# Kernel optimization log

Measured on AMD Instinct MI355X. Metric: run time of the kernel, lower is better.

Reference implementation:

```python
import jax, jax.numpy as jnp
import numpy as np

B, S, D = 128, 144, 1024  # batch, grid tokens (12x12), d_model
GRID = 12


def _relative_position(grid_size):
    # Reconstructs get_grids_pos for a grid_size x grid_size grid of unit cells
    # (x_min = cell col/row index, x_max = x_min + 1), standard grid-feature layout.
    x = jnp.arange(grid_size, dtype=jnp.float32)
    px_min = jnp.repeat(x, grid_size)          # (S,) varies slowly (rows)
    py_min = jnp.tile(x, grid_size)            # (S,) varies fast (cols)
    px_max = px_min + 1.0
    py_max = py_min + 1.0
    cx = (px_min + px_max) * 0.5
    cy = (py_min + py_max) * 0.5
    w = px_max - px_min + 1.0                  # == 2 everywhere
    h = py_max - py_min + 1.0
    eps = 1e-10
    dx = jnp.log(jnp.maximum(jnp.abs((cx[:, None] - cx[None, :]) / w[:, None]), eps))
    dy = jnp.log(jnp.maximum(jnp.abs((cy[:, None] - cy[None, :]) / h[:, None]), eps))
    dw = jnp.log(w[:, None] / w[None, :])
    dh = jnp.log(h[:, None] / h[None, :])
    return jnp.stack([dx, dy, dw, dh], axis=-1)  # (S, S, 4)


def setup_inputs() -> dict:
    key = jax.random.key(0)
    ks = jax.random.split(key, 12)
    std = 0.02
    return {
        "query": jax.random.normal(ks[0], (B, S, D), jnp.float32),
        "key":   jax.random.normal(ks[1], (B, S, D), jnp.float32),
        "value": jax.random.normal(ks[2], (B, S, D), jnp.float32),
        # Linear weights stored as (in, out): y = x @ W + b
        "Wq": jax.random.normal(ks[3], (D, D), jnp.float32) * std,
        "bq": jnp.zeros((D,), jnp.float32),
        "Wk": jax.random.normal(ks[4], (D, D), jnp.float32) * std,
        "bk": jnp.zeros((D,), jnp.float32),
        "Wv": jax.random.normal(ks[5], (D, D), jnp.float32) * std,
        "bv": jnp.zeros((D,), jnp.float32),
        "Wl": jax.random.normal(ks[6], (4, D), jnp.float32) * std,
        "bl": jnp.zeros((D,), jnp.float32),
        "w_g": jax.random.normal(ks[7], (S, D, 1), jnp.float32) * std,
    }


def reference(query, key, value, Wq, bq, Wk, bk, Wv, bv, Wl, bl, w_g):
    d_model = query.shape[-1]
    scale = d_model ** (-0.5)
    act = jax.nn.relu  # get_activation_function() assumed relu; dropout=0 (eval)

    q = act(query @ Wq + bq)   # (B,S,D)
    k = act(key @ Wk + bk)
    v = act(value @ Wv + bv)

    attn = jnp.einsum('bid,bjd->bij', q, k) * scale  # (B,S,S)

    seq = value.shape[1]
    pos = _relative_position(int(round(seq ** 0.5)))  # (S,S,4)
    rel = act(pos @ Wl + bl)                          # (S,S,D)
    # torch.matmul(rela_pos, w_g): row i of the grid uses w_g[i]
    bias = act(jnp.einsum('ijd,id->ij', rel, w_g[..., 0]))  # (S,S)

    attn = jax.nn.softmax(attn + bias[None, :, :], axis=-1)
    return jnp.einsum('bij,bjd->bid', attn, v)
```

## Files before the change

### kernel.cpp

```cpp
#include <hip/hip_runtime.h>
#include <hip/hip_bf16.h>
#include <stdint.h>

#define SS 144
#define DD 1024
#define NB 128
#define SP 160
#define SCALE 0.03125f

typedef __attribute__((ext_vector_type(8))) short short8;
typedef __attribute__((ext_vector_type(4))) float floatx4;
typedef unsigned short u16;

#define MFMA(a, b, c) __builtin_amdgcn_mfma_f32_16x16x32_bf16((a), (b), (c), 0, 0, 0)

__device__ __forceinline__ u16 f2bf(float f) {
    union { float f; unsigned int i; } v; v.f = f;
    unsigned int r = v.i + 0x7fff + ((v.i >> 16) & 1);
    return (u16)(r >> 16);
}
__device__ __forceinline__ short8 pack8(float4 a, float4 b) {
    short8 r;
    r[0] = (short)f2bf(a.x); r[1] = (short)f2bf(a.y);
    r[2] = (short)f2bf(a.z); r[3] = (short)f2bf(a.w);
    r[4] = (short)f2bf(b.x); r[5] = (short)f2bf(b.y);
    r[6] = (short)f2bf(b.z); r[7] = (short)f2bf(b.w);
    return r;
}

__device__ __forceinline__ void gload16(u16* lds, const u16* g) {
    __builtin_amdgcn_global_load_lds(
        (__attribute__((address_space(1))) void*)g,
        (__attribute__((address_space(3))) void*)lds, 16, 0, 0);
}

__global__ __launch_bounds__(256) void convert_k(const float* __restrict__ X,
                                                 u16* __restrict__ O, int nchunk) {
    for (int c = blockIdx.x * 256 + threadIdx.x; c < nchunk; c += gridDim.x * 256) {
        size_t i = (size_t)c * 8;
        float4 a = *(const float4*)(X + i);
        float4 b = *(const float4*)(X + i + 4);
        *(short8*)(O + i) = pack8(a, b);
    }
}

__global__ void transpose_w_k(const float* __restrict__ Wq, const float* __restrict__ Wk,
                              const float* __restrict__ Wv, u16* __restrict__ WT) {
    __shared__ u16 t[32][33];
    int z = blockIdx.z;
    const float* W = z == 0 ? Wq : (z == 1 ? Wk : Wv);
    u16* O = WT + (size_t)z * DD * DD;
    int bn = blockIdx.x * 32, bk = blockIdx.y * 32;
    int tx = threadIdx.x & 31, ty = threadIdx.x >> 5;
    for (int r = ty; r < 32; r += 8) t[r][tx] = f2bf(W[(size_t)(bk + r) * DD + bn + tx]);
    __syncthreads();
    for (int r = ty; r < 32; r += 8) O[(size_t)(bn + r) * DD + bk + tx] = t[tx][r];
}

__global__ void bias_k(const float* __restrict__ Wl, const float* __restrict__ bl,
                       const float* __restrict__ wg, float* __restrict__ biasb) {
    int ij = blockIdx.x;
    int i = ij / SS, j = ij - i * SS;
    int lane = threadIdx.x;
    int ri = i / 12, ci = i - ri * 12, rj = j / 12, cj = j - rj * 12;
    float dx = logf(fmaxf(fabsf((float)(ri - rj)) * 0.5f, 1e-10f));
    float dy = logf(fmaxf(fabsf((float)(ci - cj)) * 0.5f, 1e-10f));
    float s = 0.f;
    for (int d = lane; d < DD; d += 64) {
        float r = dx * Wl[d] + dy * Wl[DD + d] + bl[d];
        r = fmaxf(r, 0.f);
        s += r * wg[(size_t)i * DD + d];
    }
    #pragma unroll
    for (int m = 32; m > 0; m >>= 1) s += __shfl_xor(s, m);
    if (lane == 0) biasb[ij] = fmaxf(s, 0.f);
}

__global__ __launch_bounds__(256) void proj_k(
    const u16* __restrict__ Xb, const u16* __restrict__ Wt,
    const float* __restrict__ bias,
    u16* __restrict__ O, u16* __restrict__ OvT, int z) {
    __shared__ __align__(16) u16 As[128 * 32];
    __shared__ __align__(16) u16 Bs[128 * 32];
    int bm = blockIdx.x, bn = blockIdx.y;
    int tid = threadIdx.x, lane = tid & 63, wv = tid >> 6;
    int wm = wv >> 1, wn = wv & 1;
    int lr = lane & 15, lq = lane >> 4;

    floatx4 zero4 = {0.f, 0.f, 0.f, 0.f};
    floatx4 acc[4][4];
    #pragma unroll
    for (int r = 0; r < 4; r++)
        #pragma unroll
        for (int c = 0; c < 4; c++) acc[r][c] = zero4;

    const u16* Abase = Xb + (size_t)bm * 128 * DD;
    const u16* Bbase = Wt + (size_t)bn * 128 * DD;

    int c0 = tid, c1 = tid + 256;
    const u16* ga0 = Abase + (size_t)(c0 >> 2) * DD + ((c0 & 3) << 3);
    const u16* ga1 = Abase + (size_t)(c1 >> 2) * DD + ((c1 & 3) << 3);
    const u16* gb0 = Bbase + (size_t)(c0 >> 2) * DD + ((c0 & 3) << 3);
    const u16* gb1 = Bbase + (size_t)(c1 >> 2) * DD + ((c1 & 3) << 3);
    u16* la0 = &As[c0 * 8];
    u16* la1 = &As[c1 * 8];
    u16* lb0 = &Bs[c0 * 8];
    u16* lb1 = &Bs[c1 * 8];

    for (int k0 = 0; k0 < DD; k0 += 32) {
        __syncthreads();
        gload16(la0, ga0 + k0);
        gload16(la1, ga1 + k0);
        gload16(lb0, gb0 + k0);
        gload16(lb1, gb1 + k0);
        __syncthreads();
        short8 a[4], b[4];
        #pragma unroll
        for (int r = 0; r < 4; r++)
            a[r] = *(const short8*)&As[(wm * 64 + r * 16 + lr) * 32 + lq * 8];
        #pragma unroll
        for (int c = 0; c < 4; c++)
            b[c] = *(const short8*)&Bs[(wn * 64 + c * 16 + lr) * 32 + lq * 8];
        #pragma unroll
        for (int r = 0; r < 4; r++)
            #pragma unroll
            for (int c = 0; c < 4; c++)
                acc[r][c] = MFMA(a[r], b[c], acc[r][c]);
    }

    int mrow0 = bm * 128 + wm * 64;
    int ncol0 = bn * 128 + wn * 64;
    if (z < 2) {
        #pragma unroll
        for (int r = 0; r < 4; r++)
            #pragma unroll
            for (int c = 0; c < 4; c++) {
                int col = ncol0 + c * 16 + lr;
                float bb = bias[col];
                #pragma unroll
                for (int i = 0; i < 4; i++) {
                    int row = mrow0 + r * 16 + lq * 4 + i;
                    O[(size_t)row * DD + col] = f2bf(fmaxf(acc[r][c][i] + bb, 0.f));
                }
            }
    } else {
        #pragma unroll
        for (int r = 0; r < 4; r++)
            #pragma unroll
            for (int c = 0; c < 4; c++) {
                int col = ncol0 + c * 16 + lr;
                float bb = bias[col];
                #pragma unroll
                for (int i = 0; i < 4; i++) {
                    int row = mrow0 + r * 16 + lq * 4 + i;
                    int bidx = row / SS;
                    int srow = row - bidx * SS;
                    OvT[((size_t)bidx * DD + col) * SP + srow] =
                        f2bf(fmaxf(acc[r][c][i] + bb, 0.f));
                }
            }
    }
}

__global__ __launch_bounds__(256) void attn_k(
    const u16* __restrict__ q, const u16* __restrict__ k,
    const float* __restrict__ biasb, u16* __restrict__ probs) {
    __shared__ float Sst[16][148];
    int it = blockIdx.x, b = blockIdx.y;
    int i0 = it * 16;
    int tid = threadIdx.x, lane = tid & 63, wv = tid >> 6;
    int lr = lane & 15, lq = lane >> 4;
    const u16* qs = q + ((size_t)b * SS + i0) * DD;
    const u16* ks = k + (size_t)b * SS * DD;

    floatx4 zero4 = {0.f, 0.f, 0.f, 0.f};
    floatx4 acc[3] = {zero4, zero4, zero4};
    int nt = (wv == 0) ? 3 : 2;

    for (int d0 = 0; d0 < DD; d0 += 32) {
        short8 a = *(const short8*)&qs[(size_t)lr * DD + d0 + lq * 8];
        #pragma unroll
        for (int m = 0; m < 3; m++) {
            if (m < nt) {
                int t = wv + m * 4;
                short8 bb = *(const short8*)&ks[(size_t)(t * 16 + lr) * DD + d0 + lq * 8];
                acc[m] = MFMA(a, bb, acc[m]);
            }
        }
    }
    for (int m = 0; m < nt; m++) {
        int t = wv + m * 4;
        #pragma unroll
        for (int i = 0; i < 4; i++) {
            int row = lq * 4 + i, col = t * 16 + lr;
            Sst[row][col] = acc[m][i] * SCALE + biasb[(i0 + row) * SS + col];
        }
    }
    __syncthreads();

    int g = tid >> 4, j = tid & 15;
    float mx = -1e30f;
    for (int c = j; c < SS; c += 16) mx = fmaxf(mx, Sst[g][c]);
    #pragma unroll
    for (int m = 1; m < 16; m <<= 1) mx = fmaxf(mx, __shfl_xor(mx, m));
    float sm = 0.f;
    float ev[9];
    int t = 0;
    for (int c = j; c < SS; c += 16, t++) { float e = expf(Sst[g][c] - mx); ev[t] = e; sm += e; }
    #pragma unroll
    for (int m = 1; m < 16; m <<= 1) sm += __shfl_xor(sm, m);
    float inv = 1.f / sm;
    u16* pr = probs + ((size_t)b * SS + i0 + g) * SP;
    t = 0;
    for (int c = j; c < SP; c += 16, t++) {
        float val = (c < SS) ? ev[t < 9 ? t : 8] * inv : 0.f;
        pr[c] = f2bf(val);
    }
}

__global__ __launch_bounds__(256) void pv_k(
    const u16* __restrict__ probs, const u16* __restrict__ vT, float* __restrict__ out) {
    int cb = blockIdx.x, it = blockIdx.y, b = blockIdx.z;
    int tid = threadIdx.x, lane = tid & 63, wv = tid >> 6;
    int lr = lane & 15, lq = lane >> 4;
    const u16* pr = probs + ((size_t)b * SS + it * 16) * SP;
    const u16* vt = vT + (size_t)b * DD * SP;
    int col0 = cb * 256 + wv * 64;

    floatx4 zero4 = {0.f, 0.f, 0.f, 0.f};
    floatx4 acc[4] = {zero4, zero4, zero4, zero4};
    for (int k0 = 0; k0 < SP; k0 += 32) {
        short8 a = *(const short8*)&pr[(size_t)lr * SP + k0 + lq * 8];
        #pragma unroll
        for (int c = 0; c < 4; c++) {
            short8 bb = *(const short8*)&vt[(size_t)(col0 + c * 16 + lr) * SP + k0 + lq * 8];
            acc[c] = MFMA(a, bb, acc[c]);
        }
    }
    #pragma unroll
    for (int c = 0; c < 4; c++)
        #pragma unroll
        for (int i = 0; i < 4; i++) {
            int row = it * 16 + lq * 4 + i, col = col0 + c * 16 + lr;
            out[((size_t)b * SS + row) * DD + col] = acc[c][i];
        }
}

extern "C" void kernel_launch(void* const* d_in, const int* in_sizes, int n_in,
                              void* d_out, int out_size, void* d_ws, size_t ws_size,
                              hipStream_t stream) {
    const float* query = (const float*)d_in[0];
    const float* key_  = (const float*)d_in[1];
    const float* value = (const float*)d_in[2];
    const float* Wq = (const float*)d_in[3];
    const float* bq = (const float*)d_in[4];
    const float* Wk = (const float*)d_in[5];
    const float* bk = (const float*)d_in[6];
    const float* Wv = (const float*)d_in[7];
    const float* bv = (const float*)d_in[8];
    const float* Wl = (const float*)d_in[9];
    const float* bl = (const float*)d_in[10];
    const float* wg = (const float*)d_in[11];

    u16* WT    = (u16*)d_ws;
    u16* Xbf   = WT + (size_t)3 * DD * DD;
    u16* q     = Xbf + (size_t)NB * SS * DD;
    u16* k     = q  + (size_t)NB * SS * DD;
    u16* vT    = k  + (size_t)NB * SS * DD;
    u16* probs = vT + (size_t)NB * DD * SP;
    float* biasb = (float*)(probs + (size_t)NB * SS * SP);

    transpose_w_k<<<dim3(32, 32, 3), 256, 0, stream>>>(Wq, Wk, Wv, WT);
    bias_k<<<dim3(SS * SS), 64, 0, stream>>>(Wl, bl, wg, biasb);

    const float* Xs[3] = {query, key_, value};
    const float* bs[3] = {bq, bk, bv};
    int nchunk = NB * SS * DD / 8;
    for (int z = 0; z < 3; z++) {
        convert_k<<<dim3(2048), 256, 0, stream>>>(Xs[z], Xbf, nchunk);
        proj_k<<<dim3(144, 8), 256, 0, stream>>>(Xbf, WT + (size_t)z * DD * DD, bs[z],
                                                 z == 0 ? q : k, vT, z);
    }
    attn_k<<<dim3(9, NB), 256, 0, stream>>>(q, k, biasb, probs);
    pv_k<<<dim3(4, 9, NB), 256, 0, stream>>>(probs, vT, (float*)d_out);
}
```

Before: 646.6 us.

## Double-buffer LDS tiles in projection GEMM and transpose LDS layout

The projection GEMM now keeps two LDS buffers per operand and issues the global-to-LDS loads for the next K slice before running the MFMAs on the current one, dropping one barrier per iteration. The LDS layout also changes to k-chunk-major (chunk index times 128 rows), so a wavefront's 16-byte fragment reads hit consecutive addresses and avoid bank conflicts. This doubles LDS use per block, which may lower occupancy. Correctness depends on gload16 being able to run asynchronously while the other buffer is read.

```diff
diff --git a/kernel.cpp b/kernel.cpp
--- a/kernel.cpp
+++ b/kernel.cpp
@@ -80,8 +80,8 @@
     const u16* __restrict__ Xb, const u16* __restrict__ Wt,
     const float* __restrict__ bias,
     u16* __restrict__ O, u16* __restrict__ OvT, int z) {
-    __shared__ __align__(16) u16 As[128 * 32];
-    __shared__ __align__(16) u16 Bs[128 * 32];
+    __shared__ __align__(16) u16 As[2][128 * 32];
+    __shared__ __align__(16) u16 Bs[2][128 * 32];
     int bm = blockIdx.x, bn = blockIdx.y;
     int tid = threadIdx.x, lane = tid & 63, wv = tid >> 6;
     int wm = wv >> 1, wn = wv & 1;
@@ -98,34 +98,42 @@
     const u16* Bbase = Wt + (size_t)bn * 128 * DD;
 
     int c0 = tid, c1 = tid + 256;
-    const u16* ga0 = Abase + (size_t)(c0 >> 2) * DD + ((c0 & 3) << 3);
-    const u16* ga1 = Abase + (size_t)(c1 >> 2) * DD + ((c1 & 3) << 3);
-    const u16* gb0 = Bbase + (size_t)(c0 >> 2) * DD + ((c0 & 3) << 3);
-    const u16* gb1 = Bbase + (size_t)(c1 >> 2) * DD + ((c1 & 3) << 3);
-    u16* la0 = &As[c0 * 8];
-    u16* la1 = &As[c1 * 8];
-    u16* lb0 = &Bs[c0 * 8];
-    u16* lb1 = &Bs[c1 * 8];
-
+    const u16* gA0 = Abase + (size_t)(c0 & 127) * DD + ((c0 >> 7) << 3);
+    const u16* gA1 = Abase + (size_t)(c1 & 127) * DD + ((c1 >> 7) << 3);
+    const u16* gB0 = Bbase + (size_t)(c0 & 127) * DD + ((c0 >> 7) << 3);
+    const u16* gB1 = Bbase + (size_t)(c1 & 127) * DD + ((c1 >> 7) << 3);
+
+    gload16(&As[0][c0 * 8], gA0);
+    gload16(&As[0][c1 * 8], gA1);
+    gload16(&Bs[0][c0 * 8], gB0);
+    gload16(&Bs[0][c1 * 8], gB1);
+    __syncthreads();
+
+    int cur = 0;
     for (int k0 = 0; k0 < DD; k0 += 32) {
-        __syncthreads();
-        gload16(la0, ga0 + k0);
-        gload16(la1, ga1 + k0);
-        gload16(lb0, gb0 + k0);
-        gload16(lb1, gb1 + k0);
-        __syncthreads();
+        int nxt = cur ^ 1;
+        if (k0 + 32 < DD) {
+            gload16(&As[nxt][c0 * 8], gA0 + k0 + 32);
+            gload16(&As[nxt][c1 * 8], gA1 + k0 + 32);
+            gload16(&Bs[nxt][c0 * 8], gB0 + k0 + 32);
+            gload16(&Bs[nxt][c1 * 8], gB1 + k0 + 32);
+        }
+        const u16* Ab = As[cur];
+        const u16* Bb = Bs[cur];
         short8 a[4], b[4];
         #pragma unroll
         for (int r = 0; r < 4; r++)
-            a[r] = *(const short8*)&As[(wm * 64 + r * 16 + lr) * 32 + lq * 8];
+            a[r] = *(const short8*)&Ab[lq * 1024 + (wm * 64 + r * 16 + lr) * 8];
         #pragma unroll
         for (int c = 0; c < 4; c++)
-            b[c] = *(const short8*)&Bs[(wn * 64 + c * 16 + lr) * 32 + lq * 8];
+            b[c] = *(const short8*)&Bb[lq * 1024 + (wn * 64 + c * 16 + lr) * 8];
         #pragma unroll
         for (int r = 0; r < 4; r++)
             #pragma unroll
             for (int c = 0; c < 4; c++)
                 acc[r][c] = MFMA(a[r], b[c], acc[r][c]);
+        __syncthreads();
+        cur = nxt;
     }
 
     int mrow0 = bm * 128 + wm * 64;
```

New measurement: 748.1 us. +15.7%, slower.

## Batch Q/K/V conversion and projection into single launches using output buffer as scratch

Applied to the files above, without the earlier changes.

Replaces the three convert-then-project launch pairs with one conversion kernel over a 3-slice grid and one projection GEMM kernel over a 3-deep z grid. The bf16 copies of query and key are staged in the output buffer, and value keeps the old workspace slot. This gives larger grids that fill the GPU better, fewer launches, and no serialization between the three projections. The grid order also changes so that the N tiles vary fastest, which should improve reuse of the A tile. The scratch use of d_out is safe only because pv_k overwrites it later.

```diff
diff --git a/kernel.cpp b/kernel.cpp
--- a/kernel.cpp
+++ b/kernel.cpp
@@ -34,8 +34,13 @@
         (__attribute__((address_space(3))) void*)lds, 16, 0, 0);
 }
 
-__global__ __launch_bounds__(256) void convert_k(const float* __restrict__ X,
-                                                 u16* __restrict__ O, int nchunk) {
+__global__ __launch_bounds__(256) void convert3_k(
+    const float* __restrict__ Xq, const float* __restrict__ Xk,
+    const float* __restrict__ Xv,
+    u16* __restrict__ Oq, u16* __restrict__ Ok, u16* __restrict__ Ov, int nchunk) {
+    int z = blockIdx.y;
+    const float* X = z == 0 ? Xq : (z == 1 ? Xk : Xv);
+    u16* O = z == 0 ? Oq : (z == 1 ? Ok : Ov);
     for (int c = blockIdx.x * 256 + threadIdx.x; c < nchunk; c += gridDim.x * 256) {
         size_t i = (size_t)c * 8;
         float4 a = *(const float4*)(X + i);
@@ -77,12 +82,17 @@
 }
 
 __global__ __launch_bounds__(256) void proj_k(
-    const u16* __restrict__ Xb, const u16* __restrict__ Wt,
-    const float* __restrict__ bias,
-    u16* __restrict__ O, u16* __restrict__ OvT, int z) {
+    const u16* __restrict__ Xq, const u16* __restrict__ Xk, const u16* __restrict__ Xv,
+    const u16* __restrict__ WT,
+    const float* __restrict__ bq, const float* __restrict__ bk, const float* __restrict__ bv,
+    u16* __restrict__ Oq, u16* __restrict__ Ok, u16* __restrict__ OvT) {
     __shared__ __align__(16) u16 As[128 * 32];
     __shared__ __align__(16) u16 Bs[128 * 32];
-    int bm = blockIdx.x, bn = blockIdx.y;
+    int z = blockIdx.z;
+    const u16* Xb = z == 0 ? Xq : (z == 1 ? Xk : Xv);
+    const u16* Wt = WT + (size_t)z * DD * DD;
+    const float* bias = z == 0 ? bq : (z == 1 ? bk : bv);
+    int bn = blockIdx.x, bm = blockIdx.y;
     int tid = threadIdx.x, lane = tid & 63, wv = tid >> 6;
     int wm = wv >> 1, wn = wv & 1;
     int lr = lane & 15, lq = lane >> 4;
@@ -131,6 +141,7 @@
     int mrow0 = bm * 128 + wm * 64;
     int ncol0 = bn * 128 + wn * 64;
     if (z < 2) {
+        u16* O = z == 0 ? Oq : Ok;
         #pragma unroll
         for (int r = 0; r < 4; r++)
             #pragma unroll
@@ -263,24 +274,23 @@
     const float* wg = (const float*)d_in[11];
 
     u16* WT    = (u16*)d_ws;
-    u16* Xbf   = WT + (size_t)3 * DD * DD;
-    u16* q     = Xbf + (size_t)NB * SS * DD;
+    u16* Xv    = WT + (size_t)3 * DD * DD;
+    u16* q     = Xv + (size_t)NB * SS * DD;
     u16* k     = q  + (size_t)NB * SS * DD;
     u16* vT    = k  + (size_t)NB * SS * DD;
     u16* probs = vT + (size_t)NB * DD * SP;
     float* biasb = (float*)(probs + (size_t)NB * SS * SP);
 
+    u16* Xq = (u16*)d_out;
+    u16* Xk = Xq + (size_t)NB * SS * DD;
+
     transpose_w_k<<<dim3(32, 32, 3), 256, 0, stream>>>(Wq, Wk, Wv, WT);
     bias_k<<<dim3(SS * SS), 64, 0, stream>>>(Wl, bl, wg, biasb);
 
-    const float* Xs[3] = {query, key_, value};
-    const float* bs[3] = {bq, bk, bv};
     int nchunk = NB * SS * DD / 8;
-    for (int z = 0; z < 3; z++) {
-        convert_k<<<dim3(2048), 256, 0, stream>>>(Xs[z], Xbf, nchunk);
-        proj_k<<<dim3(144, 8), 256, 0, stream>>>(Xbf, WT + (size_t)z * DD * DD, bs[z],
-                                                 z == 0 ? q : k, vT, z);
-    }
+    convert3_k<<<dim3(1024, 3), 256, 0, stream>>>(query, key_, value, Xq, Xk, Xv, nchunk);
+    proj_k<<<dim3(8, 144, 3), 256, 0, stream>>>(Xq, Xk, Xv, WT, bq, bk, bv, q, k, vT);
+
     attn_k<<<dim3(9, NB), 256, 0, stream>>>(q, k, biasb, probs);
     pv_k<<<dim3(4, 9, NB), 256, 0, stream>>>(probs, vT, (float*)d_out);
 }
```

Result: faster. 622.1 us (-3.8%).
